# Kernel tuning notes

Hardware: AMD Instinct MI355X
Metric: run time of the kernel (lower is better)

## Reference

```python
import jax, jax.numpy as jnp
import numpy as np

N_EXAMPLES = 10  # hardcoded repeat_interleave(10) in the source

def setup_inputs() -> dict:
    key = jax.random.key(0)
    k1, k2, k3, k4 = jax.random.split(key, 4)
    B, L, S, H = 8, 256, 512, 1024
    return {
        "output": jax.random.normal(k1, (B * N_EXAMPLES, L, H), dtype=jnp.float32),
        "context0": jax.random.normal(k2, (B * N_EXAMPLES, L, H), dtype=jnp.float32),
        "context1": jax.random.normal(k3, (B, S, H), dtype=jnp.float32),
        "mask": jnp.zeros((B * N_EXAMPLES, L), dtype=bool),
        "W_out": jax.random.normal(k4, (H, 3 * H), dtype=jnp.float32) * 0.02,
        "b_out": jnp.zeros((H,), dtype=jnp.float32),
    }

def reference(output, context0, context1, mask, W_out, b_out):
    # output, context0: [B*10, L, H]; context1: [B, S, H]
    # NOTE: in the torch source, `attn.data.masked_fill(mask, -inf)` is NOT
    # in-place and its result is discarded, so the mask has no effect on the
    # math. We reproduce that faithfully: `mask` is unused.
    del mask
    set_ctx = jnp.repeat(context1, N_EXAMPLES, axis=0)  # [B*10, S, H]
    # example-attention branch: bmm -> softmax -> bmm
    ex_attn = jax.nn.softmax(jnp.einsum('bld,bsd->bls', output, context0), axis=-1)  # [B*10, L, L]
    # set-attention branch: bmm -> softmax -> bmm
    set_attn = jax.nn.softmax(jnp.einsum('bld,bsd->bls', output, set_ctx), axis=-1)  # [B*10, L, S]
    ex_c = jnp.einsum('bls,bsd->bld', ex_attn, context0)   # [B*10, L, H]
    set_c = jnp.einsum('bls,bsd->bld', set_attn, set_ctx)  # [B*10, L, H]
    all_info = jnp.concatenate([output, ex_c, set_c], axis=-1)  # [B*10, L, 3H]
    out = jnp.tanh(jnp.einsum('blk,hk->blh', all_info, W_out) + b_out)  # [B*10, L, H]
    return (out, ex_attn, set_attn)
```

## Files before the change

### kernel.cpp

```cpp
#include <hip/hip_runtime.h>
#include <stdint.h>
#include <math.h>

typedef unsigned short u16;
typedef __attribute__((ext_vector_type(8))) short short8;
typedef __attribute__((ext_vector_type(4))) float floatx4;

__device__ __forceinline__ u16 f32_to_bf16(float f) {
    union { float f; uint32_t u; } v; v.f = f;
    uint32_t r = v.u + 0x7FFF + ((v.u >> 16) & 1);
    return (u16)(r >> 16);
}
__device__ __forceinline__ float bf16_to_f32(u16 h) {
    union { uint32_t u; float f; } v; v.u = ((uint32_t)h) << 16; return v.f;
}

__device__ __forceinline__ void gl_lds16(const u16* g, u16* l) {
    __builtin_amdgcn_global_load_lds(
        (const __attribute__((address_space(1))) void*)g,
        (__attribute__((address_space(3))) void*)l, 16, 0, 0);
}


__global__ void split_kernel(const float4* __restrict__ x, ushort4* __restrict__ hi,
                             ushort4* __restrict__ lo, long n4) {
    long i = (long)blockIdx.x * blockDim.x + threadIdx.x;
    if (i >= n4) return;
    float4 v = x[i];
    ushort4 h, l;
    h.x = f32_to_bf16(v.x); l.x = f32_to_bf16(v.x - bf16_to_f32(h.x));
    h.y = f32_to_bf16(v.y); l.y = f32_to_bf16(v.y - bf16_to_f32(h.y));
    h.z = f32_to_bf16(v.z); l.z = f32_to_bf16(v.z - bf16_to_f32(h.z));
    h.w = f32_to_bf16(v.w); l.w = f32_to_bf16(v.w - bf16_to_f32(h.w));
    hi[i] = h; lo[i] = l;
}

__global__ void conv_kernel(const float4* __restrict__ x, ushort4* __restrict__ hi, long n4) {
    long i = (long)blockIdx.x * blockDim.x + threadIdx.x;
    if (i >= n4) return;
    float4 v = x[i];
    ushort4 h;
    h.x = f32_to_bf16(v.x); h.y = f32_to_bf16(v.y);
    h.z = f32_to_bf16(v.z); h.w = f32_to_bf16(v.w);
    hi[i] = h;
}

__global__ void transpose_u16(const u16* __restrict__ src, u16* __restrict__ dst,
                              int R, int C) {
    __shared__ u16 tile[32][34];
    long base = (long)blockIdx.z * R * C;
    int c0 = blockIdx.x * 32, r0 = blockIdx.y * 32;
    #pragma unroll
    for (int i = threadIdx.y; i < 32; i += 8)
        tile[i][threadIdx.x] = src[base + (long)(r0 + i) * C + c0 + threadIdx.x];
    __syncthreads();
    #pragma unroll
    for (int i = threadIdx.y; i < 32; i += 8)
        dst[base + (long)(c0 + i) * R + r0 + threadIdx.x] = tile[threadIdx.x][i];
}

template <int VPT>
__global__ void softmax_rows(float* __restrict__ data, u16* __restrict__ outb) {
    int row = blockIdx.x * 4 + (threadIdx.x >> 6);
    int lane = threadIdx.x & 63;
    long base = (long)row * (VPT * 64) + lane;
    float v[VPT];
    #pragma unroll
    for (int i = 0; i < VPT; ++i) v[i] = data[base + i * 64];
    float m = v[0];
    #pragma unroll
    for (int i = 1; i < VPT; ++i) m = fmaxf(m, v[i]);
    #pragma unroll
    for (int off = 32; off > 0; off >>= 1) m = fmaxf(m, __shfl_xor(m, off, 64));
    float s = 0.f;
    #pragma unroll
    for (int i = 0; i < VPT; ++i) { v[i] = __expf(v[i] - m); s += v[i]; }
    #pragma unroll
    for (int off = 32; off > 0; off >>= 1) s += __shfl_xor(s, off, 64);
    float inv = 1.0f / s;
    #pragma unroll
    for (int i = 0; i < VPT; ++i) {
        float r = v[i] * inv;
        data[base + i * 64] = r;
        outb[base + i * 64] = f32_to_bf16(r);
    }
}

struct GemmP {
    const u16* A[3];
    const u16* B[3];
    const u16* B2[3];
    long strideAb, strideBb, strideB2b, strideCb, strideC2b;
    int bdiv, bdiv2, kshift, kmask, nt, lda, ldb, ldb2, ldc, ldc2, mode;
    int gx, gy, nx1;
    float* Cf; float* Cf2; u16* Cb; const float* bias;
};

__global__ __launch_bounds__(512, 2) void gemm_bt8(GemmP p) {
    __shared__ u16 As[32768];
    __shared__ u16 Bs[32768];
    const int tid  = threadIdx.x;
    const int lane = tid & 63;
    const int wave = tid >> 6;
    const int quad = lane >> 4;
    const int l15  = lane & 15;
    const int wr   = wave >> 2;
    const int wc   = wave & 3;

    const int f  = blockIdx.x;
    const int Tx = gridDim.x >> 3;
    const int t  = (f & 7) * Tx + (f >> 3);
    const int n  = t % p.gx;
    const int r  = t / p.gx;
    const int m0 = (r % p.gy) * 256;
    const int bz = r / p.gy;

    const u16* Bsegs[3];
    int ldb, ldc, nn, bdv;
    long bstr, cstr;
    float* Cf;
    if (n < p.nx1) {
        Bsegs[0] = p.B[0]; Bsegs[1] = p.B[1]; Bsegs[2] = p.B[2];
        ldb = p.ldb; ldc = p.ldc; bstr = p.strideBb; cstr = p.strideCb;
        Cf = p.Cf; bdv = p.bdiv; nn = n;
    } else {
        Bsegs[0] = p.B2[0]; Bsegs[1] = p.B2[1]; Bsegs[2] = p.B2[2];
        ldb = p.ldb2; ldc = p.ldc2; bstr = p.strideB2b; cstr = p.strideC2b;
        Cf = p.Cf2; bdv = p.bdiv2; nn = n - p.nx1;
    }
    const int n0 = nn * 256;

    const long aoff = (long)bz * p.strideAb + (long)m0 * p.lda;
    const long boff = (long)(bz / bdv) * bstr + (long)n0 * ldb;

    const int srow = tid >> 2;
    const int sgc  = ((tid & 3) ^ ((srow >> 1) & 3)) * 8;

    const int rA = wr * 128 + l15;
    const u16* pA = As + rA * 32 + ((quad ^ ((rA >> 1) & 3)) * 8);
    const int rB = wc * 64 + l15;
    const u16* pB = Bs + rB * 32 + ((quad ^ ((rB >> 1) & 3)) * 8);

    const int nt = p.nt;

    auto stA = [&](int kt, int kk) {
        if (kt < nt) {
            const int seg = kt >> p.kshift;
            const u16* g = p.A[seg] + aoff + (long)srow * p.lda
                         + (((kt & p.kmask) << 6) + kk * 32 + sgc);
            u16* d = &As[((((kt & 1) << 1) | kk) << 13) + tid * 8];
            gl_lds16(g, d);
            gl_lds16(g + (long)128 * p.lda, d + 4096);
        }
    };
    auto stB = [&](int kt, int kk) {
        if (kt < nt) {
            const int seg = kt >> p.kshift;
            const u16* g = Bsegs[seg] + boff + (long)srow * ldb
                         + (((kt & p.kmask) << 6) + kk * 32 + sgc);
            u16* d = &Bs[((((kt & 1) << 1) | kk) << 13) + tid * 8];
            gl_lds16(g, d);
            gl_lds16(g + (long)128 * ldb, d + 4096);
        }
    };

    floatx4 acc[8][4];
    #pragma unroll
    for (int i = 0; i < 8; ++i)
        #pragma unroll
        for (int j = 0; j < 4; ++j)
            acc[i][j] = (floatx4){0.f, 0.f, 0.f, 0.f};

    stA(0, 0); stB(0, 0); stA(0, 1); stB(0, 1); stA(1, 0); stB(1, 0);
    asm volatile("s_waitcnt vmcnt(4)" ::: "memory");
    __builtin_amdgcn_s_barrier();

    short8 af[4], bf[4];

#define QPHASE(SO, MH, LOADB, STAGE)                                        \
    {                                                                       \
        _Pragma("unroll")                                                   \
        for (int mi = 0; mi < 4; ++mi)                                      \
            af[mi] = *(const short8*)(pA + (SO) + (MH) * 2048 + mi * 512);  \
        if (LOADB) {                                                        \
            _Pragma("unroll")                                               \
            for (int ni = 0; ni < 4; ++ni)                                  \
                bf[ni] = *(const short8*)(pB + (SO) + ni * 512);            \
        }                                                                   \
        STAGE;                                                              \
        __builtin_amdgcn_s_barrier();                                       \
        asm volatile("s_waitcnt lgkmcnt(0)" ::: "memory");                  \
        __builtin_amdgcn_sched_barrier(0);                                  \
        __builtin_amdgcn_s_setprio(1);                                      \
        _Pragma("unroll")                                                   \
        for (int mi = 0; mi < 4; ++mi)                                      \
            _Pragma("unroll")                                               \
            for (int ni = 0; ni < 4; ++ni)                                  \
                acc[(MH) * 4 + mi][ni] =                                    \
                    __builtin_amdgcn_mfma_f32_16x16x32_bf16(                \
                        af[mi], bf[ni], acc[(MH) * 4 + mi][ni], 0, 0, 0);   \
        __builtin_amdgcn_s_setprio(0);                                      \
        __builtin_amdgcn_sched_barrier(0);                                  \
    }

    for (int kt = 0; kt < nt; ++kt) {
        const int so0 = (kt & 1) << 14;
        const int so1 = so0 + 8192;
        QPHASE(so0, 0, true,  stA(kt + 1, 1));
        __builtin_amdgcn_s_barrier();
        QPHASE(so0, 1, false, stB(kt + 1, 1));
        __builtin_amdgcn_s_barrier();
        QPHASE(so1, 0, true,  stA(kt + 2, 0));
        __builtin_amdgcn_s_barrier();
        QPHASE(so1, 1, false, stB(kt + 2, 0));
        if (kt + 2 < nt) {
            asm volatile("s_waitcnt vmcnt(4)" ::: "memory");
        } else {
            asm volatile("s_waitcnt vmcnt(0)" ::: "memory");
        }
        __builtin_amdgcn_s_barrier();
    }
#undef QPHASE

    const long coff = (long)bz * cstr;
    const int rb = m0 + wr * 128 + quad * 4;
    const int cb = n0 + wc * 64 + l15;
    if (p.mode == 2) {
        #pragma unroll
        for (int ni = 0; ni < 4; ++ni) {
            const float bv = p.bias[cb + ni * 16];
            #pragma unroll
            for (int mi = 0; mi < 8; ++mi)
                #pragma unroll
                for (int j = 0; j < 4; ++j)
                    Cf[coff + (long)(rb + mi * 16 + j) * ldc + cb + ni * 16] =
                        tanhf(acc[mi][ni][j] + bv);
        }
    } else if (p.mode == 0) {
        #pragma unroll
        for (int ni = 0; ni < 4; ++ni)
            #pragma unroll
            for (int mi = 0; mi < 8; ++mi)
                #pragma unroll
                for (int j = 0; j < 4; ++j)
                    Cf[coff + (long)(rb + mi * 16 + j) * ldc + cb + ni * 16] =
                        acc[mi][ni][j];
    } else {
        #pragma unroll
        for (int ni = 0; ni < 4; ++ni)
            #pragma unroll
            for (int mi = 0; mi < 8; ++mi)
                #pragma unroll
                for (int j = 0; j < 4; ++j)
                    p.Cb[coff + (long)(rb + mi * 16 + j) * ldc + cb + ni * 16] =
                        f32_to_bf16(acc[mi][ni][j]);
    }
}

extern "C" void kernel_launch(void* const* d_in, const int* in_sizes, int n_in,
                              void* d_out, int out_size, void* d_ws, size_t ws_size,
                              hipStream_t stream) {
    const int BT = 80, L = 256, S = 512, H = 1024;
    const long NO    = (long)BT * L * H;
    const long NC1   = (long)8 * S * H;
    const long NW    = (long)H * 3 * H;
    const long NEXA  = (long)BT * L * L;
    const long NSETA = (long)BT * L * S;

    const float* X    = (const float*)d_in[0];
    const float* C0   = (const float*)d_in[1];
    const float* C1   = (const float*)d_in[2];
    const float* Wf   = (const float*)d_in[4];
    const float* bias = (const float*)d_in[5];

    float* out  = (float*)d_out;
    float* exa  = out + NO;
    float* seta = exa + NEXA;

    char* wsb = (char*)d_ws;
    size_t off = 0;
    auto alloc = [&](long nbytes) -> void* {
        void* p = (void*)(wsb + off);
        off += ((size_t)nbytes + 255) & ~(size_t)255;
        return p;
    };
    u16* Xhi  = (u16*)alloc(NO * 2);
    u16* Xlo  = (u16*)alloc(NO * 2);
    u16* C0hi = (u16*)alloc(NO * 2);
    u16* C0lo = (u16*)alloc(NO * 2);
    u16* C1hi = (u16*)alloc(NC1 * 2);
    u16* C1lo = (u16*)alloc(NC1 * 2);
    u16* Wb   = (u16*)alloc(NW * 2);
    u16* exab = (u16*)alloc(NEXA * 2);
    u16* setab= (u16*)alloc(NSETA * 2);
    u16* C0T = C0lo;
    u16* C1T = C1lo;
    u16* exc = Xlo;
    u16* setc = C0hi;

    split_kernel<<<(int)(NO / 4 / 256), 256, 0, stream>>>((const float4*)X, (ushort4*)Xhi, (ushort4*)Xlo, NO / 4);
    split_kernel<<<(int)(NO / 4 / 256), 256, 0, stream>>>((const float4*)C0, (ushort4*)C0hi, (ushort4*)C0lo, NO / 4);
    split_kernel<<<(int)(NC1 / 4 / 256), 256, 0, stream>>>((const float4*)C1, (ushort4*)C1hi, (ushort4*)C1lo, NC1 / 4);
    conv_kernel<<<(int)(NW / 4 / 256), 256, 0, stream>>>((const float4*)Wf, (ushort4*)Wb, NW / 4);

    {
        GemmP p{};
        p.A[0] = Xhi;  p.A[1] = Xlo;  p.A[2] = Xhi;
        p.B[0]  = C0hi; p.B[1]  = C0hi; p.B[2]  = C0lo;
        p.B2[0] = C1hi; p.B2[1] = C1hi; p.B2[2] = C1lo;
        p.strideAb = (long)L * H;
        p.strideBb = (long)L * H;  p.strideB2b = (long)S * H;
        p.strideCb = (long)L * L;  p.strideC2b = (long)L * S;
        p.bdiv = 1; p.bdiv2 = 10;
        p.kshift = 4; p.kmask = 15; p.nt = 48;
        p.lda = H; p.ldb = H; p.ldb2 = H;
        p.ldc = L; p.ldc2 = S; p.mode = 0;
        p.gx = 3; p.gy = 1; p.nx1 = 1;
        p.Cf = exa; p.Cf2 = seta;
        gemm_bt8<<<dim3(3 * 1 * BT, 1, 1), 512, 0, stream>>>(p);
    }
    softmax_rows<4><<<BT * L / 4, 256, 0, stream>>>(exa, exab);
    softmax_rows<8><<<BT * L / 4, 256, 0, stream>>>(seta, setab);

    transpose_u16<<<dim3(H / 32, L / 32, BT), dim3(32, 8), 0, stream>>>(C0hi, C0T, L, H);
    transpose_u16<<<dim3(H / 32, S / 32, 8), dim3(32, 8), 0, stream>>>(C1hi, C1T, S, H);

    {
        GemmP p{};
        p.A[0] = exab; p.B[0] = C0T;
        p.strideAb = (long)L * L; p.strideBb = (long)H * L; p.strideCb = (long)L * H;
        p.bdiv = 1; p.kshift = 2; p.kmask = 3; p.nt = 4;
        p.lda = L; p.ldb = L; p.ldc = H; p.mode = 1;
        p.gx = 4; p.gy = 1; p.nx1 = 4;
        p.Cb = exc;
        gemm_bt8<<<dim3(4 * 1 * BT, 1, 1), 512, 0, stream>>>(p);
    }
    {
        GemmP p{};
        p.A[0] = setab; p.B[0] = C1T;
        p.strideAb = (long)L * S; p.strideBb = (long)H * S; p.strideCb = (long)L * H;
        p.bdiv = 10; p.kshift = 3; p.kmask = 7; p.nt = 8;
        p.lda = S; p.ldb = S; p.ldc = H; p.mode = 1;
        p.gx = 4; p.gy = 1; p.nx1 = 4;
        p.Cb = setc;
        gemm_bt8<<<dim3(4 * 1 * BT, 1, 1), 512, 0, stream>>>(p);
    }
    {
        GemmP p{};
        p.A[0] = Xhi; p.A[1] = exc; p.A[2] = setc;
        p.B[0] = Wb;  p.B[1] = Wb + 1024; p.B[2] = Wb + 2048;
        p.strideAb = 0; p.strideBb = 0; p.strideCb = 0;
        p.bdiv = 1; p.kshift = 4; p.kmask = 15; p.nt = 48;
        p.lda = H; p.ldb = 3 * H; p.ldc = H; p.mode = 2;
        p.gx = 4; p.gy = BT * L / 256; p.nx1 = 4;
        p.Cf = out; p.bias = bias;
        gemm_bt8<<<dim3(4 * (BT * L / 256), 1, 1), 512, 0, stream>>>(p);
    }
}
```

Before: 775.0 us.

## Use simpler 128x128-tile GEMM kernel for context and output projection GEMMs

Adds a new gemm_bt kernel with 256 threads, 128x128 tiles, and a single-buffered LDS loop over K segments. The two attention-context GEMMs and the final output projection now use it instead of the 256x256 double-buffered gemm_bt8. For the small context GEMMs this gives four times as many workgroups, which should fill the GPU better. The price is less operand reuse per tile and no overlap between global loads and MFMA work. The old gemm_bt8 also gets per-segment base pointers computed once up front, but it is now used only by the score GEMM.

```diff
diff --git a/kernel.cpp b/kernel.cpp
--- a/kernel.cpp
+++ b/kernel.cpp
@@ -91,28 +91,28 @@
     const u16* B[3];
     const u16* B2[3];
     long strideAb, strideBb, strideB2b, strideCb, strideC2b;
-    int bdiv, bdiv2, kshift, kmask, nt, lda, ldb, ldb2, ldc, ldc2, mode;
+    int bdiv, bdiv2, nseg, Kper, kshift, kmask, nt, lda, ldb, ldb2, ldc, ldc2, mode;
     int gx, gy, nx1;
     float* Cf; float* Cf2; u16* Cb; const float* bias;
 };
 
-__global__ __launch_bounds__(512, 2) void gemm_bt8(GemmP p) {
-    __shared__ u16 As[32768];
-    __shared__ u16 Bs[32768];
+__global__ __launch_bounds__(256) void gemm_bt(GemmP p) {
+    __shared__ u16 As[128 * 64];
+    __shared__ u16 Bs[128 * 64];
     const int tid  = threadIdx.x;
     const int lane = tid & 63;
     const int wave = tid >> 6;
     const int quad = lane >> 4;
     const int l15  = lane & 15;
-    const int wr   = wave >> 2;
-    const int wc   = wave & 3;
+    const int wm = (wave & 1) * 64;
+    const int wn = (wave >> 1) * 64;
 
     const int f  = blockIdx.x;
     const int Tx = gridDim.x >> 3;
     const int t  = (f & 7) * Tx + (f >> 3);
     const int n  = t % p.gx;
     const int r  = t / p.gx;
-    const int m0 = (r % p.gy) * 256;
+    const int m0 = (r % p.gy) * 128;
     const int bz = r / p.gy;
 
     const u16* Bsegs[3];
@@ -128,13 +128,141 @@
         ldb = p.ldb2; ldc = p.ldc2; bstr = p.strideB2b; cstr = p.strideC2b;
         Cf = p.Cf2; bdv = p.bdiv2; nn = n - p.nx1;
     }
-    const int n0 = nn * 256;
+    const int n0 = nn * 128;
+
+    const int stg_r8 = tid >> 3;
+    const int stg_c  = ((tid & 7) ^ (stg_r8 & 7)) * 8;
+    const int xorl   = l15 & 7;
+
+    floatx4 acc[4][4];
+    #pragma unroll
+    for (int i = 0; i < 4; ++i)
+        #pragma unroll
+        for (int j = 0; j < 4; ++j)
+            acc[i][j] = (floatx4){0.f, 0.f, 0.f, 0.f};
 
     const long aoff = (long)bz * p.strideAb + (long)m0 * p.lda;
     const long boff = (long)(bz / bdv) * bstr + (long)n0 * ldb;
 
+    for (int seg = 0; seg < p.nseg; ++seg) {
+        const u16* Ag = p.A[seg] + aoff;
+        const u16* Bg = Bsegs[seg] + boff;
+        for (int k0 = 0; k0 < p.Kper; k0 += 64) {
+            __syncthreads();
+            #pragma unroll
+            for (int i = 0; i < 4; ++i) {
+                const int rr = i * 32 + stg_r8;
+                gl_lds16(Ag + (long)rr * p.lda + k0 + stg_c, &As[(i * 256 + tid) * 8]);
+            }
+            #pragma unroll
+            for (int i = 0; i < 4; ++i) {
+                const int rr = i * 32 + stg_r8;
+                gl_lds16(Bg + (long)rr * ldb + k0 + stg_c, &Bs[(i * 256 + tid) * 8]);
+            }
+            __syncthreads();
+            #pragma unroll
+            for (int kk = 0; kk < 2; ++kk) {
+                const int cs = ((kk * 4 + quad) ^ xorl) * 8;
+                short8 af[4], bfr[4];
+                #pragma unroll
+                for (int i = 0; i < 4; ++i)
+                    af[i] = *(const short8*)&As[(wm + i * 16 + l15) * 64 + cs];
+                #pragma unroll
+                for (int i = 0; i < 4; ++i)
+                    bfr[i] = *(const short8*)&Bs[(wn + i * 16 + l15) * 64 + cs];
+                #pragma unroll
+                for (int mi = 0; mi < 4; ++mi)
+                    #pragma unroll
+                    for (int ni = 0; ni < 4; ++ni)
+                        acc[mi][ni] = __builtin_amdgcn_mfma_f32_16x16x32_bf16(
+                            af[mi], bfr[ni], acc[mi][ni], 0, 0, 0);
+            }
+        }
+    }
+
+    const long coff = (long)bz * cstr;
+    const int rb = m0 + wm + quad * 4;
+    const int cbase = n0 + wn + l15;
+    if (p.mode == 2) {
+        #pragma unroll
+        for (int ni = 0; ni < 4; ++ni) {
+            const float bv = p.bias[cbase + ni * 16];
+            #pragma unroll
+            for (int mi = 0; mi < 4; ++mi)
+                #pragma unroll
+                for (int j = 0; j < 4; ++j)
+                    Cf[coff + (long)(rb + mi * 16 + j) * ldc + cbase + ni * 16] =
+                        tanhf(acc[mi][ni][j] + bv);
+        }
+    } else if (p.mode == 0) {
+        #pragma unroll
+        for (int ni = 0; ni < 4; ++ni)
+            #pragma unroll
+            for (int mi = 0; mi < 4; ++mi)
+                #pragma unroll
+                for (int j = 0; j < 4; ++j)
+                    Cf[coff + (long)(rb + mi * 16 + j) * ldc + cbase + ni * 16] =
+                        acc[mi][ni][j];
+    } else {
+        #pragma unroll
+        for (int ni = 0; ni < 4; ++ni)
+            #pragma unroll
+            for (int mi = 0; mi < 4; ++mi)
+                #pragma unroll
+                for (int j = 0; j < 4; ++j)
+                    p.Cb[coff + (long)(rb + mi * 16 + j) * ldc + cbase + ni * 16] =
+                        f32_to_bf16(acc[mi][ni][j]);
+    }
+}
+
+__global__ __launch_bounds__(512, 2) void gemm_bt8(GemmP p) {
+    __shared__ u16 As[32768];
+    __shared__ u16 Bs[32768];
+    const int tid  = threadIdx.x;
+    const int lane = tid & 63;
+    const int wave = tid >> 6;
+    const int quad = lane >> 4;
+    const int l15  = lane & 15;
+    const int wr   = wave >> 2;
+    const int wc   = wave & 3;
+
+    const int f  = blockIdx.x;
+    const int Tx = gridDim.x >> 3;
+    const int t  = (f & 7) * Tx + (f >> 3);
+    const int n  = t % p.gx;
+    const int r  = t / p.gx;
+    const int m0 = (r % p.gy) * 256;
+    const int bz = r / p.gy;
+
+    const u16 *B0, *B1, *B2p;
+    int ldb, ldc, nn, bdv;
+    long bstr, cstr;
+    float* Cf;
+    if (n < p.nx1) {
+        B0 = p.B[0]; B1 = p.B[1]; B2p = p.B[2];
+        ldb = p.ldb; ldc = p.ldc; bstr = p.strideBb; cstr = p.strideCb;
+        Cf = p.Cf; bdv = p.bdiv; nn = n;
+    } else {
+        B0 = p.B2[0]; B1 = p.B2[1]; B2p = p.B2[2];
+        ldb = p.ldb2; ldc = p.ldc2; bstr = p.strideB2b; cstr = p.strideC2b;
+        Cf = p.Cf2; bdv = p.bdiv2; nn = n - p.nx1;
+    }
+    const int n0 = nn * 256;
+
+    const long aoff = (long)bz * p.strideAb + (long)m0 * p.lda;
+    const long boff = (long)(bz / bdv) * bstr + (long)n0 * ldb;
+
     const int srow = tid >> 2;
     const int sgc  = ((tid & 3) ^ ((srow >> 1) & 3)) * 8;
+
+    const u16* a0 = p.A[0] + aoff + (long)srow * p.lda + sgc;
+    const u16* a1 = p.A[1] + aoff + (long)srow * p.lda + sgc;
+    const u16* a2 = p.A[2] + aoff + (long)srow * p.lda + sgc;
+    const u16* b0 = B0 + boff + (long)srow * ldb + sgc;
+    const u16* b1 = B1 + boff + (long)srow * ldb + sgc;
+    const u16* b2 = B2p + boff + (long)srow * ldb + sgc;
+    const long aStep128 = (long)128 * p.lda;
+    const long bStep128 = (long)128 * ldb;
 
     const int rA = wr * 128 + l15;
     const u16* pA = As + rA * 32 + ((quad ^ ((rA >> 1) & 3)) * 8);
@@ -146,21 +274,21 @@
     auto stA = [&](int kt, int kk) {
         if (kt < nt) {
             const int seg = kt >> p.kshift;
-            const u16* g = p.A[seg] + aoff + (long)srow * p.lda
-                         + (((kt & p.kmask) << 6) + kk * 32 + sgc);
+            const u16* base = (seg == 0) ? a0 : ((seg == 1) ? a1 : a2);
+            const u16* g = base + (((kt & p.kmask) << 6) + kk * 32);
             u16* d = &As[((((kt & 1) << 1) | kk) << 13) + tid * 8];
             gl_lds16(g, d);
-            gl_lds16(g + (long)128 * p.lda, d + 4096);
+            gl_lds16(g + aStep128, d + 4096);
         }
     };
     auto stB = [&](int kt, int kk) {
         if (kt < nt) {
             const int seg = kt >> p.kshift;
-            const u16* g = Bsegs[seg] + boff + (long)srow * ldb
-                         + (((kt & p.kmask) << 6) + kk * 32 + sgc);
+            const u16* base = (seg == 0) ? b0 : ((seg == 1) ? b1 : b2);
+            const u16* g = base + (((kt & p.kmask) << 6) + kk * 32);
             u16* d = &Bs[((((kt & 1) << 1) | kk) << 13) + tid * 8];
             gl_lds16(g, d);
-            gl_lds16(g + (long)128 * ldb, d + 4096);
+            gl_lds16(g + bStep128, d + 4096);
         }
     };
 
@@ -329,31 +457,28 @@
         GemmP p{};
         p.A[0] = exab; p.B[0] = C0T;
         p.strideAb = (long)L * L; p.strideBb = (long)H * L; p.strideCb = (long)L * H;
-        p.bdiv = 1; p.kshift = 2; p.kmask = 3; p.nt = 4;
-        p.lda = L; p.ldb = L; p.ldc = H; p.mode = 1;
-        p.gx = 4; p.gy = 1; p.nx1 = 4;
+        p.bdiv = 1; p.nseg = 1; p.Kper = L; p.lda = L; p.ldb = L; p.ldc = H; p.mode = 1;
+        p.gx = 8; p.gy = 2; p.nx1 = 8;
         p.Cb = exc;
-        gemm_bt8<<<dim3(4 * 1 * BT, 1, 1), 512, 0, stream>>>(p);
+        gemm_bt<<<dim3(8 * 2 * BT, 1, 1), 256, 0, stream>>>(p);
     }
     {
         GemmP p{};
         p.A[0] = setab; p.B[0] = C1T;
         p.strideAb = (long)L * S; p.strideBb = (long)H * S; p.strideCb = (long)L * H;
-        p.bdiv = 10; p.kshift = 3; p.kmask = 7; p.nt = 8;
-        p.lda = S; p.ldb = S; p.ldc = H; p.mode = 1;
-        p.gx = 4; p.gy = 1; p.nx1 = 4;
+        p.bdiv = 10; p.nseg = 1; p.Kper = S; p.lda = S; p.ldb = S; p.ldc = H; p.mode = 1;
+        p.gx = 8; p.gy = 2; p.nx1 = 8;
         p.Cb = setc;
-        gemm_bt8<<<dim3(4 * 1 * BT, 1, 1), 512, 0, stream>>>(p);
+        gemm_bt<<<dim3(8 * 2 * BT, 1, 1), 256, 0, stream>>>(p);
     }
     {
         GemmP p{};
         p.A[0] = Xhi; p.A[1] = exc; p.A[2] = setc;
         p.B[0] = Wb;  p.B[1] = Wb + 1024; p.B[2] = Wb + 2048;
         p.strideAb = 0; p.strideBb = 0; p.strideCb = 0;
-        p.bdiv = 1; p.kshift = 4; p.kmask = 15; p.nt = 48;
-        p.lda = H; p.ldb = 3 * H; p.ldc = H; p.mode = 2;
-        p.gx = 4; p.gy = BT * L / 256; p.nx1 = 4;
+        p.bdiv = 1; p.nseg = 3; p.Kper = H; p.lda = H; p.ldb = 3 * H; p.ldc = H; p.mode = 2;
+        p.gx = 8; p.gy = BT * L / 128; p.nx1 = 8;
         p.Cf = out; p.bias = bias;
-        gemm_bt8<<<dim3(4 * (BT * L / 256), 1, 1), 512, 0, stream>>>(p);
-    }
-}
+        gemm_bt<<<dim3(8 * (BT * L / 128), 1, 1), 256, 0, stream>>>(p);
+    }
+}
```

New measurement: 868.7 us. +12.1%, slower.
